# Performance work log

Measured on AMD Instinct MI355X. Metric: run time of the kernel, lower is better.

## Reference

```python
import jax, jax.numpy as jnp
import numpy as np

N, D, E, H, K = 16384, 256, 8, 512, 2


def setup_inputs() -> dict:
    key = jax.random.key(0)
    ks = jax.random.split(key, 5)
    inputs = jax.random.normal(ks[0], (N, D), dtype=jnp.float32)
    Wg = jax.random.normal(ks[1], (D, E), dtype=jnp.float32) * 0.05
    w1 = jax.random.normal(ks[2], (E, D, H), dtype=jnp.float32) * 0.05
    b1 = jnp.zeros((E, H), dtype=jnp.float32)
    w2 = jax.random.normal(ks[3], (E, H, D), dtype=jnp.float32) * 0.05
    b2 = jnp.zeros((E, D), dtype=jnp.float32)
    return {"inputs": inputs, "Wg": Wg, "w1": w1, "b1": b1, "w2": w2, "b2": b2}


def reference(inputs, Wg, w1, b1, w2, b2):
    # gate + top-k routing (softmax over the selected logits only, as in the torch code)
    gate_logits = inputs @ Wg                       # [N, E]
    topw, topi = jax.lax.top_k(gate_logits, K)      # [N, K]
    topw = jax.nn.softmax(topw.astype(jnp.float32), axis=1).astype(inputs.dtype)
    # combine weights scattered back into a dense [N, E] matrix (dispatch/combine)
    combine = jnp.zeros((N, E), dtype=inputs.dtype)
    combine = combine.at[jnp.arange(N)[:, None], topi].add(topw)  # [N, E]
    # expert MLP (Linear -> GELU(exact) -> Linear), computed per expert and
    # combined with the sparse routing weights (pool='sum')
    h = jax.nn.gelu(jnp.einsum('nd,edh->neh', inputs, w1) + b1[None], approximate=False)  # [N,E,H]
    y = jnp.einsum('neh,ehd->ned', h, w2) + b2[None]                                      # [N,E,D]
    return jnp.einsum('ne,ned->nd', combine, y)                                           # [N,D]
```

## Files before the change

### kernel.cpp

```cpp
#include <hip/hip_runtime.h>

#define NTOK 16384
#define DIM 256
#define NEXP 8
#define HID 512
#define CAP 5120
#define CSTRIDE 16

typedef unsigned short ushort_t;
typedef short bf16x8 __attribute__((ext_vector_type(8)));
typedef float f32x4 __attribute__((ext_vector_type(4)));
typedef float f32x16 __attribute__((ext_vector_type(16)));

static __device__ __forceinline__ ushort_t f2bf(float f) {
    unsigned int u = __float_as_uint(f);
    unsigned int r = (u + 0x7FFFu + ((u >> 16) & 1u)) >> 16;
    return (ushort_t)r;
}
static __device__ __forceinline__ float bf2f(ushort_t u) {
    unsigned int x = ((unsigned int)u) << 16;
    return __uint_as_float(x);
}
static __device__ __forceinline__ float gelu_fast(float v) {
    float v2 = v * v;
    float u = v * __builtin_fmaf(v2, -0.1029407079f, -2.3022090196f);
    float e = __builtin_amdgcn_exp2f(u);
    return v * __builtin_amdgcn_rcpf(1.0f + e);
}

__global__ void k_transpose(const float* __restrict__ w1, const float* __restrict__ w2,
                            ushort_t* __restrict__ w1t, ushort_t* __restrict__ w2t,
                            int* __restrict__ counts) {
    __shared__ ushort_t tile[64][72];
    if (blockIdx.x == 0 && threadIdx.x < NEXP * CSTRIDE) counts[threadIdx.x] = 0;
    int b = blockIdx.x;
    const float* src; ushort_t* dst; int R, C, e, t;
    if (b < 256) { e = b >> 5; t = b & 31; src = w1; dst = w1t + e * DIM * HID; R = DIM; C = HID; }
    else { b -= 256; e = b >> 5; t = b & 31; src = w2; dst = w2t + e * DIM * HID; R = HID; C = DIM; }
    size_t ebase = (size_t)e * DIM * HID;
    int tilesC = C >> 6;
    int rt = t / tilesC, ct = t % tilesC;
    for (int i = 0; i < 16; i++) {
        int flat = i * 256 + threadIdx.x;
        int lr = flat >> 6, lc = flat & 63;
        tile[lr][lc] = f2bf(src[ebase + (size_t)(rt * 64 + lr) * C + ct * 64 + lc]);
    }
    __syncthreads();
    for (int i = 0; i < 16; i++) {
        int flat = i * 256 + threadIdx.x;
        int lr = flat >> 6, lc = flat & 63;
        dst[(ct * 64 + lr) * R + rt * 64 + lc] = tile[lc][lr];
    }
}

__global__ void k_router(const float* __restrict__ X, const float* __restrict__ Wg,
                         int* counts, int* tok_list, int* inv_idx, float* inv_w,
                         ushort_t* __restrict__ Xb) {
    __shared__ float xs[64][257];
    __shared__ float lg[64][8];
    __shared__ int te0[64], te1[64], lo0[64], lo1[64];
    __shared__ float tw0[64], tw1[64];
    __shared__ int lcnt[NEXP], gbase[NEXP];
    int tid = threadIdx.x;
    int tok0 = blockIdx.x * 64;
    if (tid < NEXP) lcnt[tid] = 0;
    for (int i = 0; i < 8; i++) {
        int flat = i * 256 + tid;
        int r = flat >> 5, c8 = (flat & 31) << 3;
        const float* row = X + (size_t)(tok0 + r) * DIM + c8;
        float4 a = *(const float4*)row;
        float4 b = *(const float4*)(row + 4);
        xs[r][c8 + 0] = a.x; xs[r][c8 + 1] = a.y; xs[r][c8 + 2] = a.z; xs[r][c8 + 3] = a.w;
        xs[r][c8 + 4] = b.x; xs[r][c8 + 5] = b.y; xs[r][c8 + 6] = b.z; xs[r][c8 + 7] = b.w;
    }
    __syncthreads();
    for (int i = 0; i < 8; i++) {
        int flat = i * 256 + tid;
        int r = flat >> 5, c8 = (flat & 31) << 3;
        ushort_t pk[8];
#pragma unroll
        for (int j = 0; j < 8; j++) pk[j] = f2bf(xs[r][c8 + j]);
        *(int4*)(Xb + (size_t)(tok0 + r) * DIM + c8) = *(const int4*)pk;
    }
    int tl = tid & 63, pair = tid >> 6;
    float l0 = 0.f, l1 = 0.f;
    for (int d = 0; d < DIM; d++) {
        float x = xs[tl][d];
        l0 += x * Wg[d * NEXP + 2 * pair];
        l1 += x * Wg[d * NEXP + 2 * pair + 1];
    }
    lg[tl][2 * pair] = l0; lg[tl][2 * pair + 1] = l1;
    __syncthreads();
    if (tid < 64) {
        float best = -1e30f; int bi = 0;
#pragma unroll
        for (int e = 0; e < NEXP; e++) { float v = lg[tid][e]; if (v > best) { best = v; bi = e; } }
        float best2 = -1e30f; int bi2 = 0;
#pragma unroll
        for (int e = 0; e < NEXP; e++) { if (e == bi) continue; float v = lg[tid][e]; if (v > best2) { best2 = v; bi2 = e; } }
        float ed = __expf(best2 - best);
        te0[tid] = bi; te1[tid] = bi2;
        tw0[tid] = 1.0f / (1.0f + ed);
        tw1[tid] = ed / (1.0f + ed);
        lo0[tid] = atomicAdd(&lcnt[bi], 1);
        lo1[tid] = atomicAdd(&lcnt[bi2], 1);
    }
    __syncthreads();
    if (tid < NEXP) gbase[tid] = atomicAdd(&counts[tid * CSTRIDE], lcnt[tid]);
    __syncthreads();
    if (tid < 64) {
        int token = tok0 + tid;
        int e0 = te0[tid], e1 = te1[tid];
        int p0 = gbase[e0] + lo0[tid]; if (p0 >= CAP) p0 = CAP - 1;
        int p1 = gbase[e1] + lo1[tid]; if (p1 >= CAP) p1 = CAP - 1;
        tok_list[e0 * CAP + p0] = token;
        tok_list[e1 * CAP + p1] = token;
        inv_idx[token * 2]     = (e0 << 16) | p0;  inv_w[token * 2]     = tw0[tid];
        inv_idx[token * 2 + 1] = (e1 << 16) | p1;  inv_w[token * 2 + 1] = tw1[tid];
    }
}

__launch_bounds__(256, 2)
__global__ void k_mlp1(const ushort_t* __restrict__ Xb, const ushort_t* __restrict__ w1t,
                       const float* __restrict__ b1,
                       const int* __restrict__ counts, const int* __restrict__ tok_list,
                       ushort_t* __restrict__ hb) {
    __shared__ ushort_t B1[128 * 264];
    int b = blockIdx.x;
    int e = b / 160;
    int rem = b % 160;
    int tile = rem >> 2, hq = rem & 3;
    int count = counts[e * CSTRIDE];
    if (count > CAP) count = CAP;
    int t0 = tile * 128;
    if (t0 >= count) return;

    int tid = threadIdx.x;
    int w = tid >> 6, l = tid & 63, m = l & 31, hi = l >> 5;

    const ushort_t* w1te = w1t + (size_t)e * DIM * HID + (size_t)hq * 128 * DIM;
#pragma unroll
    for (int i = 0; i < 16; i++) {
        int flat = i * 256 + tid;
        int hr = flat >> 5, c8 = (flat & 31) << 3;
        *(int4*)(B1 + hr * 264 + c8) = *(const int4*)(w1te + hr * DIM + c8);
    }
    int arow = t0 + 32 * w + m;
    int ci = (arow < count) ? arow : (count - 1);
    int atok = tok_list[e * CAP + ci];
    const ushort_t* xrow = Xb + (size_t)atok * DIM;
    bf16x8 xf[16];
#pragma unroll
    for (int ks = 0; ks < 16; ks++)
        xf[ks] = *(const bf16x8*)(xrow + ks * 16 + hi * 8);
    __syncthreads();

    f32x16 acc[4];
#pragma unroll
    for (int i = 0; i < 4; i++) acc[i] = (f32x16)(0.0f);
#pragma unroll
    for (int ks = 0; ks < 16; ks++) {
        bf16x8 xk = xf[ks];
#pragma unroll
        for (int cf = 0; cf < 4; cf++) {
            bf16x8 wfr = *(const bf16x8*)(B1 + (cf * 32 + m) * 264 + ks * 16 + hi * 8);
            acc[cf] = __builtin_amdgcn_mfma_f32_32x32x16_bf16(wfr, xk, acc[cf], 0, 0, 0);
        }
    }
    if (arow < count) {
        ushort_t* hrow = hb + ((size_t)e * CAP + arow) * HID + hq * 128;
#pragma unroll
        for (int cf = 0; cf < 4; cf++) {
#pragma unroll
            for (int rg = 0; rg < 4; rg++) {
                int hoff = cf * 32 + 8 * rg + 4 * hi;
                float4 bv = *(const float4*)(b1 + e * HID + hq * 128 + hoff);
                ushort4 pk;
                pk.x = f2bf(gelu_fast(acc[cf][rg * 4 + 0] + bv.x));
                pk.y = f2bf(gelu_fast(acc[cf][rg * 4 + 1] + bv.y));
                pk.z = f2bf(gelu_fast(acc[cf][rg * 4 + 2] + bv.z));
                pk.w = f2bf(gelu_fast(acc[cf][rg * 4 + 3] + bv.w));
                *(ushort4*)(hrow + hoff) = pk;
            }
        }
    }
}

__launch_bounds__(256, 2)
__global__ void k_mlp2(const ushort_t* __restrict__ hb, const ushort_t* __restrict__ w2t,
                       const float* __restrict__ b2,
                       const int* __restrict__ counts, ushort_t* __restrict__ yb) {
    __shared__ ushort_t B2[64 * 520];
    int b = blockIdx.x;
    int e = b / 160;
    int rem = b % 160;
    int tile = rem >> 2, dq = rem & 3;
    int count = counts[e * CSTRIDE];
    if (count > CAP) count = CAP;
    int t0 = tile * 128;
    if (t0 >= count) return;

    int tid = threadIdx.x;
    int w = tid >> 6, l = tid & 63, m = l & 31, hi = l >> 5;

    const ushort_t* w2te = w2t + (size_t)e * DIM * HID + (size_t)dq * 64 * HID;
#pragma unroll
    for (int i = 0; i < 16; i++) {
        int flat = i * 256 + tid;
        int dr = flat >> 6, c8 = (flat & 63) << 3;
        *(int4*)(B2 + dr * 520 + c8) = *(const int4*)(w2te + dr * HID + c8);
    }
    int arow = t0 + 32 * w + m;
    int ci = (arow < count) ? arow : (count - 1);
    const ushort_t* hrow = hb + ((size_t)e * CAP + ci) * HID;
    __syncthreads();

    f32x16 acc[2];
    acc[0] = (f32x16)(0.0f); acc[1] = (f32x16)(0.0f);
#pragma unroll
    for (int kh = 0; kh < 2; kh++) {
        bf16x8 hf[16];
#pragma unroll
        for (int ks = 0; ks < 16; ks++)
            hf[ks] = *(const bf16x8*)(hrow + kh * 256 + ks * 16 + hi * 8);
#pragma unroll
        for (int ks = 0; ks < 16; ks++) {
            bf16x8 hk = hf[ks];
#pragma unroll
            for (int cf = 0; cf < 2; cf++) {
                bf16x8 wfr = *(const bf16x8*)(B2 + (cf * 32 + m) * 520 + kh * 256 + ks * 16 + hi * 8);
                acc[cf] = __builtin_amdgcn_mfma_f32_32x32x16_bf16(wfr, hk, acc[cf], 0, 0, 0);
            }
        }
    }
    if (arow < count) {
        ushort_t* yrow = yb + ((size_t)e * CAP + arow) * DIM + dq * 64;
#pragma unroll
        for (int cf = 0; cf < 2; cf++) {
#pragma unroll
            for (int rg = 0; rg < 4; rg++) {
                int doff = cf * 32 + 8 * rg + 4 * hi;
                float4 bv = *(const float4*)(b2 + e * DIM + dq * 64 + doff);
                ushort4 pk;
                pk.x = f2bf(acc[cf][rg * 4 + 0] + bv.x);
                pk.y = f2bf(acc[cf][rg * 4 + 1] + bv.y);
                pk.z = f2bf(acc[cf][rg * 4 + 2] + bv.z);
                pk.w = f2bf(acc[cf][rg * 4 + 3] + bv.w);
                *(ushort4*)(yrow + doff) = pk;
            }
        }
    }
}

__global__ void k_combine(const ushort_t* __restrict__ yb, const int* __restrict__ inv_idx,
                          const float* __restrict__ inv_w, float* __restrict__ out) {
    int tid = threadIdx.x;
    int n = blockIdx.x * 8 + (tid >> 5);
    int l32 = tid & 31, c8 = l32 << 3;
    int i0 = inv_idx[2 * n], i1 = inv_idx[2 * n + 1];
    float w0 = inv_w[2 * n], w1 = inv_w[2 * n + 1];
    size_t r0 = (size_t)(i0 >> 16) * CAP + (i0 & 0xFFFF);
    size_t r1 = (size_t)(i1 >> 16) * CAP + (i1 & 0xFFFF);
    int4 v0 = *(const int4*)(yb + r0 * DIM + c8);
    int4 v1 = *(const int4*)(yb + r1 * DIM + c8);
    ushort_t* p0 = (ushort_t*)&v0;
    ushort_t* p1 = (ushort_t*)&v1;
    float4 oa, ob;
    oa.x = w0 * bf2f(p0[0]) + w1 * bf2f(p1[0]);
    oa.y = w0 * bf2f(p0[1]) + w1 * bf2f(p1[1]);
    oa.z = w0 * bf2f(p0[2]) + w1 * bf2f(p1[2]);
    oa.w = w0 * bf2f(p0[3]) + w1 * bf2f(p1[3]);
    ob.x = w0 * bf2f(p0[4]) + w1 * bf2f(p1[4]);
    ob.y = w0 * bf2f(p0[5]) + w1 * bf2f(p1[5]);
    ob.z = w0 * bf2f(p0[6]) + w1 * bf2f(p1[6]);
    ob.w = w0 * bf2f(p0[7]) + w1 * bf2f(p1[7]);
    float4* op = (float4*)(out + (size_t)n * DIM + c8);
    op[0] = oa; op[1] = ob;
}

extern "C" void kernel_launch(void* const* d_in, const int* in_sizes, int n_in,
                              void* d_out, int out_size, void* d_ws, size_t ws_size,
                              hipStream_t stream) {
    const float* X  = (const float*)d_in[0];
    const float* Wg = (const float*)d_in[1];
    const float* w1 = (const float*)d_in[2];
    const float* b1 = (const float*)d_in[3];
    const float* w2 = (const float*)d_in[4];
    const float* b2 = (const float*)d_in[5];

    char* ws = (char*)d_ws;
    size_t off = 0;
    int* counts = (int*)(ws + off);        off = 1024;
    int* tok_list = (int*)(ws + off);      off += (size_t)NEXP * CAP * 4;
    int* inv_idx = (int*)(ws + off);       off += (size_t)NTOK * 2 * 4;
    float* inv_w = (float*)(ws + off);     off += (size_t)NTOK * 2 * 4;
    ushort_t* w1t = (ushort_t*)(ws + off); off += (size_t)NEXP * DIM * HID * 2;
    ushort_t* w2t = (ushort_t*)(ws + off); off += (size_t)NEXP * DIM * HID * 2;
    ushort_t* Xb = (ushort_t*)(ws + off);  off += (size_t)NTOK * DIM * 2;
    ushort_t* hb = (ushort_t*)(ws + off);  off += (size_t)NEXP * CAP * HID * 2;
    ushort_t* yb = (ushort_t*)(ws + off);  off += (size_t)NEXP * CAP * DIM * 2;

    k_transpose<<<512, 256, 0, stream>>>(w1, w2, w1t, w2t, counts);
    k_router<<<256, 256, 0, stream>>>(X, Wg, counts, tok_list, inv_idx, inv_w, Xb);
    k_mlp1<<<NEXP * 40 * 4, 256, 0, stream>>>(Xb, w1t, b1, counts, tok_list, hb);
    k_mlp2<<<NEXP * 40 * 4, 256, 0, stream>>>(hb, w2t, b2, counts, yb);
    k_combine<<<2048, 256, 0, stream>>>(yb, inv_idx, inv_w, (float*)d_out);
}
```

Before: 169.6 us.

## Retile expert MLP kernels to 256-token tiles with two row groups per wave

Both expert GEMM kernels now process 256 tokens per block, with each wave handling two 32-row groups so every LDS weight fragment feeds two MFMAs. k_mlp1 also narrows its hidden slice to 64 columns, halving its LDS tile, and raises launch bounds to allow 4 blocks per SM. Activations are streamed per K-chunk instead of preloaded into registers. The aim is to cut LDS weight reads and weight reloads per token and raise occupancy, at the cost of fewer blocks for mlp2 and more per-thread accumulator registers.

```diff
diff --git a/kernel.cpp b/kernel.cpp
--- a/kernel.cpp
+++ b/kernel.cpp
@@ -9,7 +9,6 @@
 
 typedef unsigned short ushort_t;
 typedef short bf16x8 __attribute__((ext_vector_type(8)));
-typedef float f32x4 __attribute__((ext_vector_type(4)));
 typedef float f32x16 __attribute__((ext_vector_type(16)));
 
 static __device__ __forceinline__ ushort_t f2bf(float f) {
@@ -120,67 +119,77 @@
     }
 }
 
-__launch_bounds__(256, 2)
+__launch_bounds__(256, 4)
 __global__ void k_mlp1(const ushort_t* __restrict__ Xb, const ushort_t* __restrict__ w1t,
                        const float* __restrict__ b1,
                        const int* __restrict__ counts, const int* __restrict__ tok_list,
                        ushort_t* __restrict__ hb) {
-    __shared__ ushort_t B1[128 * 264];
+    __shared__ ushort_t B1[64 * 264];
     int b = blockIdx.x;
     int e = b / 160;
     int rem = b % 160;
-    int tile = rem >> 2, hq = rem & 3;
+    int tile = rem >> 3, hq = rem & 7;
     int count = counts[e * CSTRIDE];
     if (count > CAP) count = CAP;
-    int t0 = tile * 128;
+    int t0 = tile * 256;
     if (t0 >= count) return;
 
     int tid = threadIdx.x;
     int w = tid >> 6, l = tid & 63, m = l & 31, hi = l >> 5;
 
-    const ushort_t* w1te = w1t + (size_t)e * DIM * HID + (size_t)hq * 128 * DIM;
-#pragma unroll
-    for (int i = 0; i < 16; i++) {
+    const ushort_t* w1te = w1t + (size_t)e * DIM * HID + (size_t)hq * 64 * DIM;
+#pragma unroll
+    for (int i = 0; i < 8; i++) {
         int flat = i * 256 + tid;
         int hr = flat >> 5, c8 = (flat & 31) << 3;
         *(int4*)(B1 + hr * 264 + c8) = *(const int4*)(w1te + hr * DIM + c8);
     }
-    int arow = t0 + 32 * w + m;
-    int ci = (arow < count) ? arow : (count - 1);
-    int atok = tok_list[e * CAP + ci];
-    const ushort_t* xrow = Xb + (size_t)atok * DIM;
-    bf16x8 xf[16];
-#pragma unroll
-    for (int ks = 0; ks < 16; ks++)
-        xf[ks] = *(const bf16x8*)(xrow + ks * 16 + hi * 8);
-    __syncthreads();
-
-    f32x16 acc[4];
-#pragma unroll
-    for (int i = 0; i < 4; i++) acc[i] = (f32x16)(0.0f);
-#pragma unroll
-    for (int ks = 0; ks < 16; ks++) {
-        bf16x8 xk = xf[ks];
-#pragma unroll
-        for (int cf = 0; cf < 4; cf++) {
-            bf16x8 wfr = *(const bf16x8*)(B1 + (cf * 32 + m) * 264 + ks * 16 + hi * 8);
-            acc[cf] = __builtin_amdgcn_mfma_f32_32x32x16_bf16(wfr, xk, acc[cf], 0, 0, 0);
+    int row0 = t0 + w * 64 + m;
+    int row1 = row0 + 32;
+    int ci0 = (row0 < count) ? row0 : (count - 1);
+    int ci1 = (row1 < count) ? row1 : (count - 1);
+    const ushort_t* x0 = Xb + (size_t)tok_list[e * CAP + ci0] * DIM + hi * 8;
+    const ushort_t* x1 = Xb + (size_t)tok_list[e * CAP + ci1] * DIM + hi * 8;
+    __syncthreads();
+
+    f32x16 acc[2][2];
+    acc[0][0] = (f32x16)(0.f); acc[0][1] = (f32x16)(0.f);
+    acc[1][0] = (f32x16)(0.f); acc[1][1] = (f32x16)(0.f);
+#pragma unroll
+    for (int kc = 0; kc < 8; kc++) {
+        bf16x8 xk0[2], xk1[2];
+        xk0[0] = *(const bf16x8*)(x0 + kc * 32);
+        xk0[1] = *(const bf16x8*)(x0 + kc * 32 + 16);
+        xk1[0] = *(const bf16x8*)(x1 + kc * 32);
+        xk1[1] = *(const bf16x8*)(x1 + kc * 32 + 16);
+#pragma unroll
+        for (int ks = 0; ks < 2; ks++) {
+#pragma unroll
+            for (int cf = 0; cf < 2; cf++) {
+                bf16x8 wfr = *(const bf16x8*)(B1 + (cf * 32 + m) * 264 + kc * 32 + ks * 16 + hi * 8);
+                acc[0][cf] = __builtin_amdgcn_mfma_f32_32x32x16_bf16(wfr, xk0[ks], acc[0][cf], 0, 0, 0);
+                acc[1][cf] = __builtin_amdgcn_mfma_f32_32x32x16_bf16(wfr, xk1[ks], acc[1][cf], 0, 0, 0);
+            }
         }
     }
-    if (arow < count) {
-        ushort_t* hrow = hb + ((size_t)e * CAP + arow) * HID + hq * 128;
-#pragma unroll
-        for (int cf = 0; cf < 4; cf++) {
-#pragma unroll
-            for (int rg = 0; rg < 4; rg++) {
-                int hoff = cf * 32 + 8 * rg + 4 * hi;
-                float4 bv = *(const float4*)(b1 + e * HID + hq * 128 + hoff);
-                ushort4 pk;
-                pk.x = f2bf(gelu_fast(acc[cf][rg * 4 + 0] + bv.x));
-                pk.y = f2bf(gelu_fast(acc[cf][rg * 4 + 1] + bv.y));
-                pk.z = f2bf(gelu_fast(acc[cf][rg * 4 + 2] + bv.z));
-                pk.w = f2bf(gelu_fast(acc[cf][rg * 4 + 3] + bv.w));
-                *(ushort4*)(hrow + hoff) = pk;
+#pragma unroll
+    for (int tg = 0; tg < 2; tg++) {
+        int arow = row0 + tg * 32;
+        if (arow < count) {
+            ushort_t* hrow = hb + ((size_t)e * CAP + arow) * HID + hq * 64;
+#pragma unroll
+            for (int cf = 0; cf < 2; cf++) {
+#pragma unroll
+                for (int rg = 0; rg < 4; rg++) {
+                    int hoff = cf * 32 + 8 * rg + 4 * hi;
+                    float4 bv = *(const float4*)(b1 + e * HID + hq * 64 + hoff);
+                    ushort4 pk;
+                    pk.x = f2bf(gelu_fast(acc[tg][cf][rg * 4 + 0] + bv.x));
+                    pk.y = f2bf(gelu_fast(acc[tg][cf][rg * 4 + 1] + bv.y));
+                    pk.z = f2bf(gelu_fast(acc[tg][cf][rg * 4 + 2] + bv.z));
+                    pk.w = f2bf(gelu_fast(acc[tg][cf][rg * 4 + 3] + bv.w));
+                    *(ushort4*)(hrow + hoff) = pk;
+                }
             }
         }
     }
@@ -192,12 +201,12 @@
                        const int* __restrict__ counts, ushort_t* __restrict__ yb) {
     __shared__ ushort_t B2[64 * 520];
     int b = blockIdx.x;
-    int e = b / 160;
-    int rem = b % 160;
+    int e = b / 80;
+    int rem = b % 80;
     int tile = rem >> 2, dq = rem & 3;
     int count = counts[e * CSTRIDE];
     if (count > CAP) count = CAP;
-    int t0 = tile * 128;
+    int t0 = tile * 256;
     if (t0 >= count) return;
 
     int tid = threadIdx.x;
@@ -210,43 +219,52 @@
         int dr = flat >> 6, c8 = (flat & 63) << 3;
         *(int4*)(B2 + dr * 520 + c8) = *(const int4*)(w2te + dr * HID + c8);
     }
-    int arow = t0 + 32 * w + m;
-    int ci = (arow < count) ? arow : (count - 1);
-    const ushort_t* hrow = hb + ((size_t)e * CAP + ci) * HID;
-    __syncthreads();
-
-    f32x16 acc[2];
-    acc[0] = (f32x16)(0.0f); acc[1] = (f32x16)(0.0f);
-#pragma unroll
-    for (int kh = 0; kh < 2; kh++) {
-        bf16x8 hf[16];
-#pragma unroll
-        for (int ks = 0; ks < 16; ks++)
-            hf[ks] = *(const bf16x8*)(hrow + kh * 256 + ks * 16 + hi * 8);
-#pragma unroll
-        for (int ks = 0; ks < 16; ks++) {
-            bf16x8 hk = hf[ks];
+    int row0 = t0 + w * 64 + m;
+    int row1 = row0 + 32;
+    int ci0 = (row0 < count) ? row0 : (count - 1);
+    int ci1 = (row1 < count) ? row1 : (count - 1);
+    const ushort_t* h0 = hb + ((size_t)e * CAP + ci0) * HID + hi * 8;
+    const ushort_t* h1 = hb + ((size_t)e * CAP + ci1) * HID + hi * 8;
+    __syncthreads();
+
+    f32x16 acc[2][2];
+    acc[0][0] = (f32x16)(0.f); acc[0][1] = (f32x16)(0.f);
+    acc[1][0] = (f32x16)(0.f); acc[1][1] = (f32x16)(0.f);
+#pragma unroll
+    for (int kc = 0; kc < 16; kc++) {
+        bf16x8 hf0[2], hf1[2];
+        hf0[0] = *(const bf16x8*)(h0 + kc * 32);
+        hf0[1] = *(const bf16x8*)(h0 + kc * 32 + 16);
+        hf1[0] = *(const bf16x8*)(h1 + kc * 32);
+        hf1[1] = *(const bf16x8*)(h1 + kc * 32 + 16);
+#pragma unroll
+        for (int ks = 0; ks < 2; ks++) {
 #pragma unroll
             for (int cf = 0; cf < 2; cf++) {
-                bf16x8 wfr = *(const bf16x8*)(B2 + (cf * 32 + m) * 520 + kh * 256 + ks * 16 + hi * 8);
-                acc[cf] = __builtin_amdgcn_mfma_f32_32x32x16_bf16(wfr, hk, acc[cf], 0, 0, 0);
+                bf16x8 wfr = *(const bf16x8*)(B2 + (cf * 32 + m) * 520 + kc * 32 + ks * 16 + hi * 8);
+                acc[0][cf] = __builtin_amdgcn_mfma_f32_32x32x16_bf16(wfr, hf0[ks], acc[0][cf], 0, 0, 0);
+                acc[1][cf] = __builtin_amdgcn_mfma_f32_32x32x16_bf16(wfr, hf1[ks], acc[1][cf], 0, 0, 0);
             }
         }
     }
-    if (arow < count) {
-        ushort_t* yrow = yb + ((size_t)e * CAP + arow) * DIM + dq * 64;
-#pragma unroll
-        for (int cf = 0; cf < 2; cf++) {
-#pragma unroll
-            for (int rg = 0; rg < 4; rg++) {
-                int doff = cf * 32 + 8 * rg + 4 * hi;
-                float4 bv = *(const float4*)(b2 + e * DIM + dq * 64 + doff);
-                ushort4 pk;
-                pk.x = f2bf(acc[cf][rg * 4 + 0] + bv.x);
-                pk.y = f2bf(acc[cf][rg * 4 + 1] + bv.y);
-                pk.z = f2bf(acc[cf][rg * 4 + 2] + bv.z);
-                pk.w = f2bf(acc[cf][rg * 4 + 3] + bv.w);
-                *(ushort4*)(yrow + doff) = pk;
+#pragma unroll
+    for (int tg = 0; tg < 2; tg++) {
+        int arow = row0 + tg * 32;
+        if (arow < count) {
+            ushort_t* yrow = yb + ((size_t)e * CAP + arow) * DIM + dq * 64;
+#pragma unroll
+            for (int cf = 0; cf < 2; cf++) {
+#pragma unroll
+                for (int rg = 0; rg < 4; rg++) {
+                    int doff = cf * 32 + 8 * rg + 4 * hi;
+                    float4 bv = *(const float4*)(b2 + e * DIM + dq * 64 + doff);
+                    ushort4 pk;
+                    pk.x = f2bf(acc[tg][cf][rg * 4 + 0] + bv.x);
+                    pk.y = f2bf(acc[tg][cf][rg * 4 + 1] + bv.y);
+                    pk.z = f2bf(acc[tg][cf][rg * 4 + 2] + bv.z);
+                    pk.w = f2bf(acc[tg][cf][rg * 4 + 3] + bv.w);
+                    *(ushort4*)(yrow + doff) = pk;
+                }
             }
         }
     }
@@ -302,7 +320,7 @@
 
     k_transpose<<<512, 256, 0, stream>>>(w1, w2, w1t, w2t, counts);
     k_router<<<256, 256, 0, stream>>>(X, Wg, counts, tok_list, inv_idx, inv_w, Xb);
-    k_mlp1<<<NEXP * 40 * 4, 256, 0, stream>>>(Xb, w1t, b1, counts, tok_list, hb);
-    k_mlp2<<<NEXP * 40 * 4, 256, 0, stream>>>(hb, w2t, b2, counts, yb);
+    k_mlp1<<<NEXP * 20 * 8, 256, 0, stream>>>(Xb, w1t, b1, counts, tok_list, hb);
+    k_mlp2<<<NEXP * 20 * 4, 256, 0, stream>>>(hb, w2t, b2, counts, yb);
     k_combine<<<2048, 256, 0, stream>>>(yb, inv_idx, inv_w, (float*)d_out);
 }
```

Measured after the change: 185.7 us. +9.5%, slower.
